# Kernel tuning notes

Measured on AMD Instinct MI355X. Metric: run time of the kernel, lower is better.

Reference implementation:

```python
import jax, jax.numpy as jnp
import numpy as np

MIN_NUMBER = -1e32


def setup_inputs() -> dict:
    key = jax.random.key(0)
    k1, k2, k3, k4, k5 = jax.random.split(key, 5)
    B, S, H, Q = 32, 2048, 2048, 1024
    rnn_out = jax.random.normal(k1, (B, S, H), dtype=jnp.float32)
    reversed_top_h_t = jax.random.normal(k2, (B, Q), dtype=jnp.float32)
    attention_mask = jnp.ones((B, S), dtype=jnp.int32)
    # parameters (scaled like default torch inits)
    Wa = jax.random.normal(k3, (Q, Q), dtype=jnp.float32) / np.sqrt(Q)
    Ua = jax.random.normal(k4, (Q, H), dtype=jnp.float32) / np.sqrt(H)   # Conv1d k=1 weight [out,in]
    Va = jax.random.normal(k5, (Q,), dtype=jnp.float32) / np.sqrt(Q)     # Conv1d q->1 weight
    return {
        "rnn_out": rnn_out,
        "reversed_top_h_t": reversed_top_h_t,
        "attention_mask": attention_mask,
        "Wa": Wa,
        "Ua": Ua,
        "Va": Va,
    }


def reference(rnn_out, reversed_top_h_t, attention_mask, Wa, Ua, Va):
    # rnn_out: [B, S, H]; reversed_top_h_t: [B, Q]; attention_mask: [B, S]
    c1 = reversed_top_h_t @ Wa.T                      # [B, Q]  (nn.Linear, no bias)
    c2 = jnp.einsum("qh,bsh->bqs", Ua, rnn_out)       # [B, Q, S] (1x1 conv over hiddens)
    c4 = jnp.tanh(c1[:, :, None] + c2)                # broadcast add + tanh
    e = jnp.einsum("q,bqs->bs", Va, c4)               # [B, S] scores (1x1 conv q->1)
    e = jnp.where(attention_mask == 0, MIN_NUMBER, e)
    a = jax.nn.softmax(e, axis=1)                     # [B, S]
    context_hidden = jnp.einsum("bsh,bs->bh", rnn_out, a)  # [B, H]
    # dropout is identity at inference (p=0)
    return context_hidden
```

## Files before the change

kernel.cpp:

```cpp
#include <hip/hip_runtime.h>
#include <hip/hip_bf16.h>

#define Bn 32
#define Sn 2048
#define Hn 2048
#define Qn 1024
#define Mn (Bn * Sn)

typedef __attribute__((ext_vector_type(8))) short bf16x8;
typedef __attribute__((ext_vector_type(4))) float f32x4;

__device__ __forceinline__ unsigned short f2bf(float x) {
  unsigned int u = __float_as_uint(x);
  unsigned int r = (u + 0x7FFFu + ((u >> 16) & 1u)) >> 16;
  return (unsigned short)r;
}

__device__ __forceinline__ float bf2f(short s) {
  return __uint_as_float(((unsigned int)(unsigned short)s) << 16);
}

__device__ __forceinline__ unsigned int cvtpk(float lo, float hi) {
  unsigned int r;
  asm("v_cvt_pk_bf16_f32 %0, %1, %2" : "=v"(r) : "v"(lo), "v"(hi));
  return r;
}

__device__ __forceinline__ void gload16(const void* g, void* l) {
  __builtin_amdgcn_global_load_lds(
      (const __attribute__((address_space(1))) unsigned int*)g,
      (__attribute__((address_space(3))) unsigned int*)l, 16, 0, 0);
}

__global__ void cvt_rnn_kernel(const float* __restrict__ in,
                               unsigned short* __restrict__ out) {
  const size_t total8 = (size_t)Mn * Hn / 8;
  size_t i = (size_t)blockIdx.x * 256 + threadIdx.x;
  const size_t stride = (size_t)gridDim.x * 256;
  for (; i < total8; i += stride) {
    float4 v0 = ((const float4*)in)[i * 2];
    float4 v1 = ((const float4*)in)[i * 2 + 1];
    union { unsigned int u[4]; bf16x8 v; } pk;
    pk.u[0] = cvtpk(v0.x, v0.y);
    pk.u[1] = cvtpk(v0.z, v0.w);
    pk.u[2] = cvtpk(v1.x, v1.y);
    pk.u[3] = cvtpk(v1.z, v1.w);
    *(bf16x8*)(out + i * 8) = pk.v;
  }
}

__global__ void c1_kernel(const float* __restrict__ rev,
                          const float* __restrict__ Wa,
                          float* __restrict__ c1) {
  int wid = (blockIdx.x * 256 + threadIdx.x) >> 6;
  int lane = threadIdx.x & 63;
  int b = wid >> 10;
  int q = wid & (Qn - 1);
  const float* rv = rev + (size_t)b * Qn;
  const float* wr = Wa + (size_t)q * Qn;
  float acc = 0.f;
#pragma unroll
  for (int k = 0; k < Qn; k += 64) acc += rv[k + lane] * wr[k + lane];
#pragma unroll
  for (int m = 32; m > 0; m >>= 1) acc += __shfl_xor(acc, m, 64);
  if (lane == 0) c1[wid] = acc;
}

__global__ void cvt_ua_kernel(const float* __restrict__ Ua,
                              unsigned short* __restrict__ out) {
  int i = blockIdx.x * 256 + threadIdx.x;
  float4 v = ((const float4*)Ua)[i];
  typedef __attribute__((ext_vector_type(4))) unsigned short u16x4;
  u16x4 o = {f2bf(v.x), f2bf(v.y), f2bf(v.z), f2bf(v.w)};
  *(u16x4*)(out + (size_t)i * 4) = o;
}

#define NKT 32

#define VMW(n)                                                                \
  do {                                                                        \
    asm volatile("s_waitcnt vmcnt(" #n ")");                                  \
    __builtin_amdgcn_sched_barrier(0);                                        \
  } while (0)
#define NOP_ ((void)0)
#define BAR __builtin_amdgcn_s_barrier()
#define LK0                                                                   \
  do {                                                                        \
    asm volatile("s_waitcnt lgkmcnt(0)");                                     \
    __builtin_amdgcn_sched_barrier(0);                                        \
  } while (0)
#define PIN __builtin_amdgcn_sched_barrier(0)

#define STAGE_A(kt, h)                                                        \
  do {                                                                        \
    int d_ = (kt) & 1;                                                        \
    gload16(aS + (size_t)((h) * 128) * Hn + (kt) * 64,                        \
            ldsA + d_ * 32768 + (h) * 16384 + wl);                            \
    gload16(aS + (size_t)((h) * 128 + 64) * Hn + (kt) * 64,                   \
            ldsA + d_ * 32768 + (h) * 16384 + 8192 + wl);                     \
  } while (0)

#define STAGE_B(kt, h)                                                        \
  do {                                                                        \
    int d_ = (kt) & 1;                                                        \
    gload16(bS + (size_t)((h) * 128) * Hn + (kt) * 64,                        \
            ldsB + d_ * 32768 + (h) * 16384 + wl);                            \
    gload16(bS + (size_t)((h) * 128 + 64) * Hn + (kt) * 64,                   \
            ldsB + d_ * 32768 + (h) * 16384 + 8192 + wl);                     \
  } while (0)

#define RD_A(dst, d, qm)                                                      \
  do {                                                                        \
    _Pragma("unroll") for (int ii = 0; ii < 4; ii++) {                        \
      dst[ii][0] = *(const bf16x8*)(ldsA + (d) * 32768 + rA +                 \
                                    ((qm) * 64 + ii * 16) * 128 + cA0);       \
      dst[ii][1] = *(const bf16x8*)(ldsA + (d) * 32768 + rA +                 \
                                    ((qm) * 64 + ii * 16) * 128 + cA1);       \
    }                                                                         \
  } while (0)

#define RD_B(d)                                                               \
  do {                                                                        \
    _Pragma("unroll") for (int jj = 0; jj < 4; jj++) {                        \
      bfr[jj][0] =                                                            \
          *(const bf16x8*)(ldsB + (d) * 32768 + rB + (jj * 16) * 128 + cA0);  \
      bfr[jj][1] =                                                            \
          *(const bf16x8*)(ldsB + (d) * 32768 + rB + (jj * 16) * 128 + cA1);  \
    }                                                                         \
  } while (0)

#define MM(qm, qn, A_)                                                        \
  do {                                                                        \
    __builtin_amdgcn_s_setprio(1);                                            \
    _Pragma("unroll") for (int ii = 0; ii < 4; ii++)                          \
        _Pragma("unroll") for (int jj = 0; jj < 2; jj++)                      \
            _Pragma("unroll") for (int ks = 0; ks < 2; ks++)                  \
                acc[(qm) * 4 + ii][(qn) * 2 + jj] =                           \
        __builtin_amdgcn_mfma_f32_16x16x32_bf16(                              \
            A_[ii][ks], bfr[(qn) * 2 + jj][ks],                               \
            acc[(qm) * 4 + ii][(qn) * 2 + jj], 0, 0, 0);                      \
    __builtin_amdgcn_s_setprio(0);                                            \
  } while (0)

#define TILE4(d, S1, S2, S3, S4, WEND)                                        \
  do {                                                                        \
    RD_A(afr0, d, 0);                                                         \
    RD_B(d);                                                                  \
    S1; BAR; LK0; MM(0, 0, afr0); BAR; PIN;                                   \
    RD_A(afr1, d, 1);                                                         \
    S2; BAR; LK0; MM(0, 1, afr0); BAR; PIN;                                   \
    S3; BAR; LK0; MM(1, 0, afr1); BAR; PIN;                                   \
    S4; BAR; LK0; MM(1, 1, afr1); WEND; BAR; PIN;                             \
  } while (0)

__global__ __launch_bounds__(512) void gemm8_kernel(
    const unsigned short* __restrict__ A, const unsigned short* __restrict__ Bm,
    const float* __restrict__ c1, const float* __restrict__ Va,
    float* __restrict__ e) {
  __shared__ __align__(128) char lds[131072];
  __shared__ float c1s[256];
  __shared__ float Vas[256];

  const int t = threadIdx.x;
  const int l = t & 63;
  const int w = t >> 6;
  const int wr = w >> 2, wc = w & 3;

  int bid = blockIdx.x;
  int swz = (bid & 7) * 128 + (bid >> 3);
  const int mtile = swz >> 2;
  const int ntile = swz & 3;
  const int m0 = mtile * 256, n0 = ntile * 256;
  const int bidx = mtile >> 3;

  const int sr = t >> 3;
  const int sj = (t & 7) ^ (sr & 7);
  const unsigned short* aS = A + (size_t)(m0 + sr) * Hn + sj * 8;
  const unsigned short* bS = Bm + (size_t)(n0 + sr) * Hn + sj * 8;
  char* ldsA = lds;
  char* ldsB = lds + 65536;
  const int wl = w * 1024;

  const int xk = l & 7;
  const int lr4 = l >> 4;
  const int cA0 = ((0 * 4 + lr4) ^ xk) * 16;
  const int cA1 = ((1 * 4 + lr4) ^ xk) * 16;
  const int rA = (wr * 128 + (l & 15)) * 128;
  const int rB = (wc * 64 + (l & 15)) * 128;

  f32x4 acc[8][4];
#pragma unroll
  for (int i = 0; i < 8; i++)
#pragma unroll
    for (int j = 0; j < 4; j++) acc[i][j] = (f32x4){0.f, 0.f, 0.f, 0.f};

  bf16x8 afr0[4][2], afr1[4][2], bfr[4][2];

  STAGE_A(0, 0);
  STAGE_A(0, 1);
  STAGE_B(0, 0);
  STAGE_B(0, 1);
  STAGE_B(1, 0);
  STAGE_B(1, 1);
  PIN;
  VMW(4);
  BAR;
  PIN;

#pragma unroll 1
  for (int it = 0; it < NKT / 2 - 1; ++it) {
    const int ko = 2 * it + 1;
    const int k2 = 2 * it + 2, k3 = 2 * it + 3;
    TILE4(0, STAGE_A(ko, 0), STAGE_A(ko, 1), STAGE_B(k2, 0), STAGE_B(k2, 1),
          VMW(4));
    TILE4(1, STAGE_A(k2, 0), STAGE_A(k2, 1), STAGE_B(k3, 0), STAGE_B(k3, 1),
          VMW(4));
  }

  TILE4(0, STAGE_A(31, 0), STAGE_A(31, 1), NOP_, NOP_, VMW(0));
  TILE4(1, NOP_, NOP_, NOP_, NOP_, NOP_);

  if (t < 256) {
    c1s[t] = c1[bidx * Qn + n0 + t];
    Vas[t] = Va[n0 + t];
  }
  __syncthreads();

#pragma unroll
  for (int i = 0; i < 8; i++) {
#pragma unroll
    for (int r = 0; r < 4; r++) {
      float sum = 0.f;
#pragma unroll
      for (int j = 0; j < 4; j++) {
        int ql = wc * 64 + j * 16 + (l & 15);
        float x = c1s[ql] + acc[i][j][r];
        float ex = __expf(2.f * x);
        sum += Vas[ql] * (1.f - 2.f / (ex + 1.f));
      }
#pragma unroll
      for (int m = 8; m > 0; m >>= 1) sum += __shfl_xor(sum, m, 16);
      if ((l & 15) == 0) {
        int row = m0 + wr * 128 + i * 16 + (l >> 4) * 4 + r;
        atomicAdd(&e[row], sum);
      }
    }
  }
}

__global__ void softmax_kernel(const float* __restrict__ e,
                               const int* __restrict__ mask,
                               float* __restrict__ a) {
  const int b = blockIdx.x;
  const int t = threadIdx.x;
  const int lane = t & 63;
  const int w = t >> 6;
  __shared__ float red[8];
  float v[8];
  float mx = -3.0e38f;
#pragma unroll
  for (int i = 0; i < 8; i++) {
    int s = i * 256 + t;
    float x = e[(size_t)b * Sn + s];
    if (mask[(size_t)b * Sn + s] == 0) x = -1e32f;
    v[i] = x;
    mx = fmaxf(mx, x);
  }
#pragma unroll
  for (int m = 32; m > 0; m >>= 1) mx = fmaxf(mx, __shfl_xor(mx, m, 64));
  if (lane == 0) red[w] = mx;
  __syncthreads();
  mx = fmaxf(fmaxf(red[0], red[1]), fmaxf(red[2], red[3]));
  float sm = 0.f;
#pragma unroll
  for (int i = 0; i < 8; i++) {
    v[i] = __expf(v[i] - mx);
    sm += v[i];
  }
#pragma unroll
  for (int m = 32; m > 0; m >>= 1) sm += __shfl_xor(sm, m, 64);
  if (lane == 0) red[4 + w] = sm;
  __syncthreads();
  sm = red[4] + red[5] + red[6] + red[7];
  float inv = 1.f / sm;
#pragma unroll
  for (int i = 0; i < 8; i++) a[(size_t)b * Sn + i * 256 + t] = v[i] * inv;
}

__global__ void ctx_bf16_kernel(const unsigned short* __restrict__ rnnbf,
                                const float* __restrict__ a,
                                float* __restrict__ out) {
  const int b = blockIdx.y;
  const int sc = blockIdx.x;
  const int t = threadIdx.x;
  __shared__ float as_[256];
  as_[t] = a[(size_t)b * Sn + sc * 256 + t];
  __syncthreads();
  float ac[8] = {0, 0, 0, 0, 0, 0, 0, 0};
  const unsigned short* base =
      rnnbf + ((size_t)b * Sn + sc * 256) * Hn + t * 8;
  for (int s = 0; s < 256; s++) {
    float wgt = as_[s];
    bf16x8 v = *(const bf16x8*)(base + (size_t)s * Hn);
#pragma unroll
    for (int k = 0; k < 8; k++) ac[k] += wgt * bf2f(v[k]);
  }
  float* o = out + (size_t)b * Hn + t * 8;
#pragma unroll
  for (int k = 0; k < 8; k++) atomicAdd(o + k, ac[k]);
}

extern "C" void kernel_launch(void* const* d_in, const int* in_sizes, int n_in,
                              void* d_out, int out_size, void* d_ws,
                              size_t ws_size, hipStream_t stream) {
  const float* rnn = (const float*)d_in[0];
  const float* rev = (const float*)d_in[1];
  const int* mask = (const int*)d_in[2];
  const float* Wa = (const float*)d_in[3];
  const float* Ua = (const float*)d_in[4];
  const float* Va = (const float*)d_in[5];

  const size_t RNBF = (size_t)Mn * Hn * 2;
  char* w = (char*)d_ws;
  unsigned short* rnnbf = (unsigned short*)w;
  unsigned short* Uabf = (unsigned short*)(w + RNBF);
  float* c1 = (float*)(w + RNBF + 4194304);
  float* e = (float*)(w + RNBF + 4194304 + 131072);
  float* a = (float*)(w + RNBF + 4194304 + 131072 + 262144);

  hipMemsetAsync(e, 0, (size_t)Mn * sizeof(float), stream);
  hipMemsetAsync(d_out, 0, (size_t)out_size * sizeof(float), stream);

  cvt_rnn_kernel<<<4096, 256, 0, stream>>>(rnn, rnnbf);
  cvt_ua_kernel<<<(Qn * Hn / 4) / 256, 256, 0, stream>>>(Ua, Uabf);
  c1_kernel<<<(Bn * Qn) / 4, 256, 0, stream>>>(rev, Wa, c1);

  gemm8_kernel<<<(Mn / 256) * (Qn / 256), 512, 0, stream>>>(rnnbf, Uabf, c1,
                                                            Va, e);
  softmax_kernel<<<Bn, 256, 0, stream>>>(e, mask, a);

  dim3 gc(8, Bn);
  ctx_bf16_kernel<<<gc, 256, 0, stream>>>(rnnbf, a, (float*)d_out);
}
```

Before: 493.9 us.

## Load B fragments directly from global into registers, halve LDS, allow two blocks per CU

The B operand (Ua in bf16) is no longer staged through LDS. Each wave loads its B fragments straight from global memory into double-buffered registers, and the finer-grained barrier/lgkmcnt schedule is replaced with one barrier per k-tile. LDS drops to 64KB and launch bounds request 2 blocks per CU, which is meant to raise occupancy and cut LDS traffic and barrier stalls. The cost is redundant global/L2 reads of B across the two wave rows and much higher register pressure, since acc plus double-buffered B fragments must fit the 2-block budget.

After: 644.0 us. +30.4%, slower.

```diff
diff --git a/kernel.cpp b/kernel.cpp
--- a/kernel.cpp
+++ b/kernel.cpp
@@ -84,11 +84,6 @@
   } while (0)
 #define NOP_ ((void)0)
 #define BAR __builtin_amdgcn_s_barrier()
-#define LK0                                                                   \
-  do {                                                                        \
-    asm volatile("s_waitcnt lgkmcnt(0)");                                     \
-    __builtin_amdgcn_sched_barrier(0);                                        \
-  } while (0)
 #define PIN __builtin_amdgcn_sched_barrier(0)
 
 #define STAGE_A(kt, h)                                                        \
@@ -100,13 +95,12 @@
             ldsA + d_ * 32768 + (h) * 16384 + 8192 + wl);                     \
   } while (0)
 
-#define STAGE_B(kt, h)                                                        \
-  do {                                                                        \
-    int d_ = (kt) & 1;                                                        \
-    gload16(bS + (size_t)((h) * 128) * Hn + (kt) * 64,                        \
-            ldsB + d_ * 32768 + (h) * 16384 + wl);                            \
-    gload16(bS + (size_t)((h) * 128 + 64) * Hn + (kt) * 64,                   \
-            ldsB + d_ * 32768 + (h) * 16384 + 8192 + wl);                     \
+#define BLOAD(kt, dst)                                                        \
+  do {                                                                        \
+    _Pragma("unroll") for (int jj = 0; jj < 4; jj++)                          \
+        _Pragma("unroll") for (int ks = 0; ks < 2; ks++)                      \
+            dst[jj][ks] = *(const bf16x8*)(bG + (size_t)((jj) * 16) * Hn +    \
+                                           (kt) * 64 + (ks) * 32);            \
   } while (0)
 
 #define RD_A(dst, d, qm)                                                      \
@@ -119,17 +113,7 @@
     }                                                                         \
   } while (0)
 
-#define RD_B(d)                                                               \
-  do {                                                                        \
-    _Pragma("unroll") for (int jj = 0; jj < 4; jj++) {                        \
-      bfr[jj][0] =                                                            \
-          *(const bf16x8*)(ldsB + (d) * 32768 + rB + (jj * 16) * 128 + cA0);  \
-      bfr[jj][1] =                                                            \
-          *(const bf16x8*)(ldsB + (d) * 32768 + rB + (jj * 16) * 128 + cA1);  \
-    }                                                                         \
-  } while (0)
-
-#define MM(qm, qn, A_)                                                        \
+#define MM(qm, qn, A_, B_)                                                    \
   do {                                                                        \
     __builtin_amdgcn_s_setprio(1);                                            \
     _Pragma("unroll") for (int ii = 0; ii < 4; ii++)                          \
@@ -137,27 +121,29 @@
             _Pragma("unroll") for (int ks = 0; ks < 2; ks++)                  \
                 acc[(qm) * 4 + ii][(qn) * 2 + jj] =                           \
         __builtin_amdgcn_mfma_f32_16x16x32_bf16(                              \
-            A_[ii][ks], bfr[(qn) * 2 + jj][ks],                               \
+            A_[ii][ks], B_[(qn) * 2 + jj][ks],                                \
             acc[(qm) * 4 + ii][(qn) * 2 + jj], 0, 0, 0);                      \
     __builtin_amdgcn_s_setprio(0);                                            \
   } while (0)
 
-#define TILE4(d, S1, S2, S3, S4, WEND)                                        \
-  do {                                                                        \
-    RD_A(afr0, d, 0);                                                         \
-    RD_B(d);                                                                  \
-    S1; BAR; LK0; MM(0, 0, afr0); BAR; PIN;                                   \
-    RD_A(afr1, d, 1);                                                         \
-    S2; BAR; LK0; MM(0, 1, afr0); BAR; PIN;                                   \
-    S3; BAR; LK0; MM(1, 0, afr1); BAR; PIN;                                   \
-    S4; BAR; LK0; MM(1, 1, afr1); WEND; BAR; PIN;                             \
-  } while (0)
-
-__global__ __launch_bounds__(512) void gemm8_kernel(
+#define TILE(d, BC, SA, SB, WEND)                                             \
+  do {                                                                        \
+    SA; PIN;                                                                  \
+    SB; PIN;                                                                  \
+    RD_A(afr, d, 0);                                                          \
+    MM(0, 0, afr, BC);                                                        \
+    MM(0, 1, afr, BC);                                                        \
+    RD_A(afr, d, 1);                                                          \
+    MM(1, 0, afr, BC);                                                        \
+    MM(1, 1, afr, BC);                                                        \
+    PIN; WEND; BAR; PIN;                                                      \
+  } while (0)
+
+__global__ __launch_bounds__(512, 2) void gemm8_kernel(
     const unsigned short* __restrict__ A, const unsigned short* __restrict__ Bm,
     const float* __restrict__ c1, const float* __restrict__ Va,
     float* __restrict__ e) {
-  __shared__ __align__(128) char lds[131072];
+  __shared__ __align__(128) char lds[65536];
   __shared__ float c1s[256];
   __shared__ float Vas[256];
 
@@ -176,9 +162,7 @@
   const int sr = t >> 3;
   const int sj = (t & 7) ^ (sr & 7);
   const unsigned short* aS = A + (size_t)(m0 + sr) * Hn + sj * 8;
-  const unsigned short* bS = Bm + (size_t)(n0 + sr) * Hn + sj * 8;
   char* ldsA = lds;
-  char* ldsB = lds + 65536;
   const int wl = w * 1024;
 
   const int xk = l & 7;
@@ -186,7 +170,9 @@
   const int cA0 = ((0 * 4 + lr4) ^ xk) * 16;
   const int cA1 = ((1 * 4 + lr4) ^ xk) * 16;
   const int rA = (wr * 128 + (l & 15)) * 128;
-  const int rB = (wc * 64 + (l & 15)) * 128;
+
+  const unsigned short* bG = Bm + (size_t)(n0 + wc * 64 + (l & 15)) * Hn +
+                             lr4 * 8;
 
   f32x4 acc[8][4];
 #pragma unroll
@@ -194,31 +180,28 @@
 #pragma unroll
     for (int j = 0; j < 4; j++) acc[i][j] = (f32x4){0.f, 0.f, 0.f, 0.f};
 
-  bf16x8 afr0[4][2], afr1[4][2], bfr[4][2];
+  bf16x8 afr[4][2], bfrE[4][2], bfrO[4][2];
 
   STAGE_A(0, 0);
   STAGE_A(0, 1);
-  STAGE_B(0, 0);
-  STAGE_B(0, 1);
-  STAGE_B(1, 0);
-  STAGE_B(1, 1);
   PIN;
-  VMW(4);
+  BLOAD(0, bfrE);
+  PIN;
+  VMW(8);
   BAR;
   PIN;
 
 #pragma unroll 1
   for (int it = 0; it < NKT / 2 - 1; ++it) {
-    const int ko = 2 * it + 1;
-    const int k2 = 2 * it + 2, k3 = 2 * it + 3;
-    TILE4(0, STAGE_A(ko, 0), STAGE_A(ko, 1), STAGE_B(k2, 0), STAGE_B(k2, 1),
-          VMW(4));
-    TILE4(1, STAGE_A(k2, 0), STAGE_A(k2, 1), STAGE_B(k3, 0), STAGE_B(k3, 1),
-          VMW(4));
-  }
-
-  TILE4(0, STAGE_A(31, 0), STAGE_A(31, 1), NOP_, NOP_, VMW(0));
-  TILE4(1, NOP_, NOP_, NOP_, NOP_, NOP_);
+    const int k1 = 2 * it + 1, k2 = 2 * it + 2;
+    TILE(0, bfrE, { STAGE_A(k1, 0); STAGE_A(k1, 1); }, BLOAD(k1, bfrO),
+         VMW(8));
+    TILE(1, bfrO, { STAGE_A(k2, 0); STAGE_A(k2, 1); }, BLOAD(k2, bfrE),
+         VMW(8));
+  }
+
+  TILE(0, bfrE, { STAGE_A(31, 0); STAGE_A(31, 1); }, BLOAD(31, bfrO), VMW(8));
+  TILE(1, bfrO, NOP_, NOP_, VMW(0));
 
   if (t < 256) {
     c1s[t] = c1[bidx * Qn + n0 + t];
```

## Switch GEMM to 32x32x16 MFMA with simpler single-buffer-ahead k-loop

Applied to the files above, without the earlier changes.

Replaces the 16x16x32 bf16 MFMA tiling with 32x32x16 MFMA, which reduces LDS fragment reads per flop and changes the accumulator layout and epilogue row mapping. It also restructures the main loop: prefetch depth drops from two B stages to one, the fine-grained vmcnt/lgkmcnt waits are removed, and each k-tile ends with a full __syncthreads. This trades better MFMA efficiency for less latency hiding of global loads and heavier synchronization.

New measurement: 659.9 us. 33.6% more time.

```diff
diff --git a/kernel.cpp b/kernel.cpp
--- a/kernel.cpp
+++ b/kernel.cpp
@@ -9,6 +9,7 @@
 
 typedef __attribute__((ext_vector_type(8))) short bf16x8;
 typedef __attribute__((ext_vector_type(4))) float f32x4;
+typedef __attribute__((ext_vector_type(16))) float f32x16;
 
 __device__ __forceinline__ unsigned short f2bf(float x) {
   unsigned int u = __float_as_uint(x);
@@ -77,18 +78,8 @@
 
 #define NKT 32
 
-#define VMW(n)                                                                \
-  do {                                                                        \
-    asm volatile("s_waitcnt vmcnt(" #n ")");                                  \
-    __builtin_amdgcn_sched_barrier(0);                                        \
-  } while (0)
 #define NOP_ ((void)0)
 #define BAR __builtin_amdgcn_s_barrier()
-#define LK0                                                                   \
-  do {                                                                        \
-    asm volatile("s_waitcnt lgkmcnt(0)");                                     \
-    __builtin_amdgcn_sched_barrier(0);                                        \
-  } while (0)
 #define PIN __builtin_amdgcn_sched_barrier(0)
 
 #define STAGE_A(kt, h)                                                        \
@@ -109,48 +100,29 @@
             ldsB + d_ * 32768 + (h) * 16384 + 8192 + wl);                     \
   } while (0)
 
-#define RD_A(dst, d, qm)                                                      \
-  do {                                                                        \
-    _Pragma("unroll") for (int ii = 0; ii < 4; ii++) {                        \
-      dst[ii][0] = *(const bf16x8*)(ldsA + (d) * 32768 + rA +                 \
-                                    ((qm) * 64 + ii * 16) * 128 + cA0);       \
-      dst[ii][1] = *(const bf16x8*)(ldsA + (d) * 32768 + rA +                 \
-                                    ((qm) * 64 + ii * 16) * 128 + cA1);       \
-    }                                                                         \
-  } while (0)
-
-#define RD_B(d)                                                               \
-  do {                                                                        \
-    _Pragma("unroll") for (int jj = 0; jj < 4; jj++) {                        \
-      bfr[jj][0] =                                                            \
-          *(const bf16x8*)(ldsB + (d) * 32768 + rB + (jj * 16) * 128 + cA0);  \
-      bfr[jj][1] =                                                            \
-          *(const bf16x8*)(ldsB + (d) * 32768 + rB + (jj * 16) * 128 + cA1);  \
-    }                                                                         \
-  } while (0)
-
-#define MM(qm, qn, A_)                                                        \
+#define RD_B_ALL(d)                                                           \
+  do {                                                                        \
+    _Pragma("unroll") for (int nj = 0; nj < 2; nj++)                          \
+        _Pragma("unroll") for (int ks = 0; ks < 4; ks++)                      \
+            bfr[nj][ks] = *(const bf16x8*)(ldsB + (d) * 32768 +               \
+                                           (rB + nj * 32) * 128 + cB[ks]);    \
+  } while (0)
+
+#define RD_A1(d, mi)                                                          \
+  do {                                                                        \
+    _Pragma("unroll") for (int ks = 0; ks < 4; ks++)                          \
+        afr[mi][ks] = *(const bf16x8*)(ldsA + (d) * 32768 +                   \
+                                       (rA + (mi) * 32) * 128 + cA[ks]);      \
+  } while (0)
+
+#define MM(mi)                                                                \
   do {                                                                        \
     __builtin_amdgcn_s_setprio(1);                                            \
-    _Pragma("unroll") for (int ii = 0; ii < 4; ii++)                          \
-        _Pragma("unroll") for (int jj = 0; jj < 2; jj++)                      \
-            _Pragma("unroll") for (int ks = 0; ks < 2; ks++)                  \
-                acc[(qm) * 4 + ii][(qn) * 2 + jj] =                           \
-        __builtin_amdgcn_mfma_f32_16x16x32_bf16(                              \
-            A_[ii][ks], bfr[(qn) * 2 + jj][ks],                               \
-            acc[(qm) * 4 + ii][(qn) * 2 + jj], 0, 0, 0);                      \
+    _Pragma("unroll") for (int ks = 0; ks < 4; ks++)                          \
+        _Pragma("unroll") for (int nj = 0; nj < 2; nj++)                      \
+            acc[mi][nj] = __builtin_amdgcn_mfma_f32_32x32x16_bf16(            \
+                afr[mi][ks], bfr[nj][ks], acc[mi][nj], 0, 0, 0);              \
     __builtin_amdgcn_s_setprio(0);                                            \
-  } while (0)
-
-#define TILE4(d, S1, S2, S3, S4, WEND)                                        \
-  do {                                                                        \
-    RD_A(afr0, d, 0);                                                         \
-    RD_B(d);                                                                  \
-    S1; BAR; LK0; MM(0, 0, afr0); BAR; PIN;                                   \
-    RD_A(afr1, d, 1);                                                         \
-    S2; BAR; LK0; MM(0, 1, afr0); BAR; PIN;                                   \
-    S3; BAR; LK0; MM(1, 0, afr1); BAR; PIN;                                   \
-    S4; BAR; LK0; MM(1, 1, afr1); WEND; BAR; PIN;                             \
   } while (0)
 
 __global__ __launch_bounds__(512) void gemm8_kernel(
@@ -181,44 +153,69 @@
   char* ldsB = lds + 65536;
   const int wl = w * 1024;
 
-  const int xk = l & 7;
-  const int lr4 = l >> 4;
-  const int cA0 = ((0 * 4 + lr4) ^ xk) * 16;
-  const int cA1 = ((1 * 4 + lr4) ^ xk) * 16;
-  const int rA = (wr * 128 + (l & 15)) * 128;
-  const int rB = (wc * 64 + (l & 15)) * 128;
-
-  f32x4 acc[8][4];
-#pragma unroll
-  for (int i = 0; i < 8; i++)
-#pragma unroll
-    for (int j = 0; j < 4; j++) acc[i][j] = (f32x4){0.f, 0.f, 0.f, 0.f};
-
-  bf16x8 afr0[4][2], afr1[4][2], bfr[4][2];
+  const int la = l & 31;
+  const int hi = l >> 5;
+  const int rA = wr * 128 + la;
+  const int rB = wc * 64 + la;
+  const int xa = rA & 7, xb = rB & 7;
+  int cA[4], cB[4];
+#pragma unroll
+  for (int ks = 0; ks < 4; ks++) {
+    cA[ks] = ((ks * 2 + hi) ^ xa) * 16;
+    cB[ks] = ((ks * 2 + hi) ^ xb) * 16;
+  }
+
+  f32x16 acc[4][2];
+#pragma unroll
+  for (int i = 0; i < 4; i++)
+#pragma unroll
+    for (int j = 0; j < 2; j++)
+#pragma unroll
+      for (int r = 0; r < 16; r++) acc[i][j][r] = 0.f;
+
+  bf16x8 afr[4][4], bfr[2][4];
 
   STAGE_A(0, 0);
   STAGE_A(0, 1);
   STAGE_B(0, 0);
   STAGE_B(0, 1);
-  STAGE_B(1, 0);
-  STAGE_B(1, 1);
   PIN;
-  VMW(4);
-  BAR;
-  PIN;
+  __syncthreads();
 
 #pragma unroll 1
-  for (int it = 0; it < NKT / 2 - 1; ++it) {
-    const int ko = 2 * it + 1;
-    const int k2 = 2 * it + 2, k3 = 2 * it + 3;
-    TILE4(0, STAGE_A(ko, 0), STAGE_A(ko, 1), STAGE_B(k2, 0), STAGE_B(k2, 1),
-          VMW(4));
-    TILE4(1, STAGE_A(k2, 0), STAGE_A(k2, 1), STAGE_B(k3, 0), STAGE_B(k3, 1),
-          VMW(4));
-  }
-
-  TILE4(0, STAGE_A(31, 0), STAGE_A(31, 1), NOP_, NOP_, VMW(0));
-  TILE4(1, NOP_, NOP_, NOP_, NOP_, NOP_);
+  for (int kt = 0; kt < NKT - 1; ++kt) {
+    const int d = kt & 1;
+    const int nt = kt + 1;
+    RD_B_ALL(d);
+    RD_A1(d, 0);
+    STAGE_B(nt, 0);
+    STAGE_B(nt, 1);
+    STAGE_A(nt, 0);
+    STAGE_A(nt, 1);
+    PIN;
+    BAR;
+    RD_A1(d, 1);
+    MM(0);
+    BAR;
+    RD_A1(d, 2);
+    MM(1);
+    BAR;
+    RD_A1(d, 3);
+    MM(2);
+    BAR;
+    MM(3);
+    __syncthreads();
+  }
+
+  RD_B_ALL(1);
+  RD_A1(1, 0);
+  RD_A1(1, 1);
+  RD_A1(1, 2);
+  RD_A1(1, 3);
+  MM(0);
+  MM(1);
+  MM(2);
+  MM(3);
 
   if (t < 256) {
     c1s[t] = c1[bidx * Qn + n0 + t];
@@ -227,22 +224,22 @@
   __syncthreads();
 
 #pragma unroll
-  for (int i = 0; i < 8; i++) {
-#pragma unroll
-    for (int r = 0; r < 4; r++) {
-      float sum = 0.f;
-#pragma unroll
-      for (int j = 0; j < 4; j++) {
-        int ql = wc * 64 + j * 16 + (l & 15);
-        float x = c1s[ql] + acc[i][j][r];
+  for (int mi = 0; mi < 4; mi++) {
+#pragma unroll
+    for (int r = 0; r < 16; r++) {
+      float s = 0.f;
+#pragma unroll
+      for (int nj = 0; nj < 2; nj++) {
+        int ql = wc * 64 + nj * 32 + la;
+        float x = c1s[ql] + acc[mi][nj][r];
         float ex = __expf(2.f * x);
-        sum += Vas[ql] * (1.f - 2.f / (ex + 1.f));
+        s += Vas[ql] * (1.f - 2.f / (ex + 1.f));
       }
 #pragma unroll
-      for (int m = 8; m > 0; m >>= 1) sum += __shfl_xor(sum, m, 16);
-      if ((l & 15) == 0) {
-        int row = m0 + wr * 128 + i * 16 + (l >> 4) * 4 + r;
-        atomicAdd(&e[row], sum);
+      for (int m = 16; m > 0; m >>= 1) s += __shfl_xor(s, m);
+      if (la == 0) {
+        int row = m0 + wr * 128 + mi * 32 + (r & 3) + 8 * (r >> 2) + 4 * hi;
+        atomicAdd(&e[row], s);
       }
     }
   }
```
